# Kernel tuning notes

Hardware: AMD Instinct MI355X
Metric: run time of the kernel (lower is better)

Reference implementation:

```python
import jax, jax.numpy as jnp
import numpy as np

B, N, C, H, P = 16, 4096, 256, 4, 64  # batch, tokens, hidden, heads, proj_size
HD = C // H  # head dim = 64
EPS = 1e-12  # torch F.normalize eps


def _l2norm(t):
    # normalize along last axis, torch-style: t / max(||t||, eps)
    n = jnp.sqrt(jnp.sum(t * t, axis=-1, keepdims=True))
    return t / jnp.maximum(n, EPS)


def setup_inputs() -> dict:
    key = jax.random.key(0)
    ks = jax.random.split(key, 12)
    s = 0.02
    return {
        "x": jax.random.normal(ks[0], (B, N, C), jnp.float32),
        "ref": jax.random.normal(ks[1], (B, N, C), jnp.float32),
        "Wq": jax.random.normal(ks[2], (C, C), jnp.float32) * s,
        "bq": jnp.zeros((C,), jnp.float32),
        "Wkvv": jax.random.normal(ks[3], (3 * C, C), jnp.float32) * s,
        "bkvv": jnp.zeros((3 * C,), jnp.float32),
        "WE": jax.random.normal(ks[4], (P, N), jnp.float32) * s,  # E and F share weights
        "bE": jnp.zeros((P,), jnp.float32),
        "Wo1": jax.random.normal(ks[5], (C // 2, C), jnp.float32) * s,
        "bo1": jnp.zeros((C // 2,), jnp.float32),
        "Wo2": jax.random.normal(ks[6], (C // 2, C), jnp.float32) * s,
        "bo2": jnp.zeros((C // 2,), jnp.float32),
        "temp": jnp.ones((H, 1, 1), jnp.float32),
        "temp2": jnp.ones((H, 1, 1), jnp.float32),
    }


def reference(x, ref, Wq, bq, Wkvv, bkvv, WE, bE, Wo1, bo1, Wo2, bo2, temp, temp2):
    b, n, c = x.shape
    hd = c // H
    # q projection -> [B,H,hd,N] (already transposed so channel dim first)
    q = (x @ Wq.T + bq).reshape(b, n, H, hd).transpose(0, 2, 3, 1)
    kvv = (ref @ Wkvv.T + bkvv).reshape(b, n, 3, H, hd).transpose(2, 0, 3, 4, 1)
    k, v_ca, v_sa = kvv[0], kvv[1], kvv[2]
    # L2 normalize over token axis (last)
    qn = _l2norm(q)
    kn = _l2norm(k)
    # ---- channel attention (XCA-style): [B,H,hd,hd]
    attn_ca = jax.nn.softmax(jnp.einsum('bhcn,bhdn->bhcd', qn, kn) * temp, axis=-1)
    x_ca = jnp.einsum('bhcd,bhdn->bhcn', attn_ca, v_ca)  # [B,H,hd,N]
    x_ca = x_ca.transpose(0, 3, 1, 2).reshape(b, n, c)   # [B,N,C]
    # ---- spatial attention with Linformer-style projection (E == F shared)
    k_proj = kn @ WE.T + bE      # [B,H,hd,P]
    v_proj = v_sa @ WE.T + bE    # [B,H,hd,P]
    attn_sa = jax.nn.softmax(jnp.einsum('bhcn,bhcp->bhnp', qn, k_proj) * temp2, axis=-1)
    x_sa = jnp.einsum('bhnp,bhcp->bhnc', attn_sa, v_proj)  # [B,H,N,hd]
    # faithful to original permute(0,3,1,2).reshape(B,N,C)
    x_sa = x_sa.transpose(0, 3, 1, 2).reshape(b, n, c)
    # output projections + concat (SA first, then CA)
    out_ca = x_ca @ Wo1.T + bo1
    out_sa = x_sa @ Wo2.T + bo2
    return jnp.concatenate((out_sa, out_ca), axis=-1)
```

## Files before the change

### kernel.cpp

```cpp
#include <hip/hip_runtime.h>
#include <hip/hip_bf16.h>

#define DI __device__ __forceinline__

constexpr int B_ = 16, N_ = 4096, C_ = 256, H_ = 4;
constexpr size_t QSZ = (size_t)4096 * 4096;
constexpr int LDW = 72;
constexpr int LDC = 136;

typedef __attribute__((ext_vector_type(8))) short bh8;
typedef __attribute__((ext_vector_type(4))) float fx4;
typedef __attribute__((address_space(1))) unsigned int gu32;
typedef __attribute__((address_space(3))) unsigned int lu32;

DI float bfu2f(unsigned short u) { return __uint_as_float(((unsigned)u) << 16); }
DI void bfu2x2(unsigned u, float& lo, float& hi) {
  lo = __uint_as_float(u << 16);
  hi = __uint_as_float(u & 0xffff0000u);
}
DI unsigned short f2bfu(float f) {
  unsigned u = __float_as_uint(f);
  unsigned r = 0x7fffu + ((u >> 16) & 1u);
  return (unsigned short)((u + r) >> 16);
}
DI void gl_lds16(const unsigned short* g, unsigned short* l) {
  __builtin_amdgcn_global_load_lds((gu32*)g, (lu32*)l, 16, 0, 0);
}

__global__ __launch_bounds__(256) void cast_xref(
    const float* __restrict__ x, const float* __restrict__ ref,
    unsigned short* __restrict__ xb, unsigned short* __restrict__ refb)
{
  const int bid = blockIdx.x;
  const float* src = (bid < 8192) ? x : ref;
  unsigned short* dst = (bid < 8192) ? xb : refb;
  const size_t base = ((size_t)(bid & 8191) * 256 + threadIdx.x) * 8;
  const float4 a = *reinterpret_cast<const float4*>(&src[base]);
  const float4 b = *reinterpret_cast<const float4*>(&src[base + 4]);
  union { uint4 v; unsigned short u[8]; } pk;
  pk.u[0] = f2bfu(a.x); pk.u[1] = f2bfu(a.y); pk.u[2] = f2bfu(a.z); pk.u[3] = f2bfu(a.w);
  pk.u[4] = f2bfu(b.x); pk.u[5] = f2bfu(b.y); pk.u[6] = f2bfu(b.z); pk.u[7] = f2bfu(b.w);
  *reinterpret_cast<uint4*>(&dst[base]) = pk.v;
}

__global__ __launch_bounds__(256) void cast_w(
    const float* __restrict__ Wq, const float* __restrict__ Wkvv,
    const float* __restrict__ Wo2, const float* __restrict__ Wo1,
    const float* __restrict__ WE, unsigned short* __restrict__ Wb,
    unsigned short* __restrict__ wEb)
{
  const int b = blockIdx.x;
  const float* src; unsigned short* dst; int lb;
  if (b < 32)       { src = Wq;   dst = Wb;          lb = b; }
  else if (b < 128) { src = Wkvv; dst = Wb + 65536;  lb = b - 32; }
  else if (b < 144) { src = Wo2;  dst = Wb + 262144; lb = b - 128; }
  else if (b < 160) { src = Wo1;  dst = Wb + 294912; lb = b - 144; }
  else              { src = WE;   dst = wEb;         lb = b - 160; }
  const size_t base = ((size_t)lb * 256 + threadIdx.x) * 8;
  const float4 a = *reinterpret_cast<const float4*>(&src[base]);
  const float4 bb = *reinterpret_cast<const float4*>(&src[base + 4]);
  union { uint4 v; unsigned short u[8]; } pk;
  pk.u[0] = f2bfu(a.x);  pk.u[1] = f2bfu(a.y);  pk.u[2] = f2bfu(a.z);  pk.u[3] = f2bfu(a.w);
  pk.u[4] = f2bfu(bb.x); pk.u[5] = f2bfu(bb.y); pk.u[6] = f2bfu(bb.z); pk.u[7] = f2bfu(bb.w);
  *reinterpret_cast<uint4*>(&dst[base]) = pk.v;
}

__global__ __launch_bounds__(256) void proj_fused(
    const unsigned short* __restrict__ xb, const unsigned short* __restrict__ refb,
    const unsigned short* __restrict__ Wball,
    const float* __restrict__ bq, const float* __restrict__ bkvv,
    unsigned short* __restrict__ qT, unsigned short* __restrict__ kvv2T,
    unsigned short* __restrict__ qtok, unsigned short* __restrict__ vtok)
{
  __shared__ unsigned short smem[32768];
  __shared__ float biasS[128];
  const int tid = threadIdx.x;
  const int lane = tid & 63, wid = tid >> 6;
  const int l15 = lane & 15, l4 = lane >> 4;
  const int wr = wid >> 1, wc = wid & 1;
  const int yt = blockIdx.y;
  const bool isq = (yt < 2);
  const unsigned short* Ab = isq ? xb : refb;
  const unsigned short* Wsrc = isq ? Wball : (Wball + 65536);
  const float* bias = isq ? bq : bkvv;
  unsigned short* outT = isq ? qT : kvv2T;
  const int j0 = (isq ? yt : (yt - 2)) * 128;
  const int pl = j0 >> 8;
  const bool writeT = isq || (pl != 1);
  const int plT = (!isq && pl == 2) ? 1 : 0;
  unsigned short* tok = isq ? qtok : ((pl == 1) ? vtok : nullptr);
  const int n0 = blockIdx.x * 128;
  const int b = blockIdx.z;
  const size_t tok0 = (size_t)b * 4096 + n0;
  const int lrow = lane >> 3, lcb = lane & 7;
  if (tid < 128) biasS[tid] = bias[j0 + tid];

  fx4 acc[4][4];
#pragma unroll
  for (int m = 0; m < 4; ++m)
#pragma unroll
    for (int n = 0; n < 4; ++n) acc[m][n] = (fx4){0.f, 0.f, 0.f, 0.f};

  auto STAGE = [&](int buf, int k0) {
    unsigned short* Wd = smem + buf * 16384;
    unsigned short* Xd = Wd + 8192;
#pragma unroll
    for (int i = 0; i < 4; ++i) {
      const int ci = i * 4 + wid;
      const int row = ci * 8 + lrow;
      const int scb = lcb ^ (row & 7);
      gl_lds16(&Wsrc[(size_t)(j0 + row) * 256 + k0 + scb * 8], &Wd[ci * 512]);
      gl_lds16(&Ab[(tok0 + row) * 256 + k0 + scb * 8], &Xd[ci * 512]);
    }
  };
  auto COMPUTE = [&](int buf) {
    const unsigned short* Ws = smem + buf * 16384;
    const unsigned short* Xs = Ws + 8192;
#pragma unroll
    for (int kk = 0; kk < 2; ++kk) {
      const int cbi = kk * 4 + l4;
      bh8 af[4], bfr[4];
#pragma unroll
      for (int m = 0; m < 4; ++m) {
        const int r = wr * 64 + m * 16 + l15;
        af[m] = *reinterpret_cast<const bh8*>(&Ws[r * 64 + ((cbi ^ (r & 7)) << 3)]);
      }
#pragma unroll
      for (int n = 0; n < 4; ++n) {
        const int r = wc * 64 + n * 16 + l15;
        bfr[n] = *reinterpret_cast<const bh8*>(&Xs[r * 64 + ((cbi ^ (r & 7)) << 3)]);
      }
#pragma unroll
      for (int m = 0; m < 4; ++m)
#pragma unroll
        for (int n = 0; n < 4; ++n)
          acc[m][n] = __builtin_amdgcn_mfma_f32_16x16x32_bf16(af[m], bfr[n], acc[m][n], 0, 0, 0);
    }
  };

  STAGE(0, 0);
  __syncthreads();
  for (int t = 0; t < 4; ++t) {
    if (t < 3) STAGE((t + 1) & 1, (t + 1) * 64);
    COMPUTE(t & 1);
    __syncthreads();
  }

  unsigned short* Co = smem;
#pragma unroll
  for (int m = 0; m < 4; ++m) {
    const int jl = wr * 64 + m * 16 + (l4 << 2);
#pragma unroll
    for (int n = 0; n < 4; ++n) {
      const int col = wc * 64 + n * 16 + l15;
#pragma unroll
      for (int r = 0; r < 4; ++r)
        Co[(jl + r) * LDC + col] = f2bfu(acc[m][n][r] + biasS[jl + r]);
    }
  }
  __syncthreads();
  if (writeT) {
#pragma unroll
    for (int c = 0; c < 8; ++c) {
      const int r = tid >> 1;
      const int colseg = (tid & 1) * 64 + c * 8;
      const uint4 v = *reinterpret_cast<const uint4*>(&Co[r * LDC + colseg]);
      const int jj = j0 + r;
      const int rowT = (plT * B_ + b) * 256 + (jj & 255);
      *reinterpret_cast<uint4*>(&outT[(size_t)rowT * N_ + n0 + colseg]) = v;
    }
  }
  if (tok) {
#pragma unroll
    for (int i = 0; i < 8; ++i) {
      const int idx = i * 256 + tid;
      const int col = idx & 127;
      const int cb = (idx >> 7) * 8;
      union { uint4 v; unsigned short u[8]; } pk;
#pragma unroll
      for (int t = 0; t < 8; ++t) pk.u[t] = Co[(cb + t) * LDC + col];
      const int jj = j0 + cb;
      const int hh = (jj >> 6) & 3, cc = jj & 63;
      *reinterpret_cast<uint4*>(
          &tok[(((size_t)b * 4 + hh) * 4096 + n0 + col) * 64 + cc]) = pk.v;
    }
  }
}

__global__ __launch_bounds__(256) void gemm_outm2(
    const unsigned short* __restrict__ Asa, const unsigned short* __restrict__ Aca,
    const unsigned short* __restrict__ Wob,
    const float* __restrict__ bo2, const float* __restrict__ bo1,
    float* __restrict__ out)
{
  __shared__ unsigned short smem[32768];
  __shared__ float biasS[128];
  const unsigned short* A = (blockIdx.z == 0) ? Asa : Aca;
  const unsigned short* Wsrc = Wob + (size_t)blockIdx.z * 32768;
  const float* bias = (blockIdx.z == 0) ? bo2 : bo1;
  const int joff = blockIdx.z * 128;
  const int tid = threadIdx.x;
  const int lane = tid & 63, wid = tid >> 6;
  const int l15 = lane & 15, l4 = lane >> 4;
  const int wr = wid >> 1, wc = wid & 1;
  const size_t m0 = (size_t)blockIdx.x * 128;
  const int lrow = lane >> 3, lcb = lane & 7;
  if (tid < 128) biasS[tid] = bias[tid];

  fx4 acc[4][4];
#pragma unroll
  for (int m = 0; m < 4; ++m)
#pragma unroll
    for (int n = 0; n < 4; ++n) acc[m][n] = (fx4){0.f, 0.f, 0.f, 0.f};

  auto STAGE = [&](int buf, int k0) {
    unsigned short* Wd = smem + buf * 16384;
    unsigned short* Xd = Wd + 8192;
#pragma unroll
    for (int i = 0; i < 4; ++i) {
      const int ci = i * 4 + wid;
      const int row = ci * 8 + lrow;
      const int scb = lcb ^ (row & 7);
      gl_lds16(&Wsrc[(size_t)row * 256 + k0 + scb * 8], &Wd[ci * 512]);
      gl_lds16(&A[(m0 + row) * 256 + k0 + scb * 8], &Xd[ci * 512]);
    }
  };
  auto COMPUTE = [&](int buf) {
    const unsigned short* Ws = smem + buf * 16384;
    const unsigned short* Xs = Ws + 8192;
#pragma unroll
    for (int kk = 0; kk < 2; ++kk) {
      const int cbi = kk * 4 + l4;
      bh8 af[4], bfr[4];
#pragma unroll
      for (int m = 0; m < 4; ++m) {
        const int r = wr * 64 + m * 16 + l15;
        af[m] = *reinterpret_cast<const bh8*>(&Xs[r * 64 + ((cbi ^ (r & 7)) << 3)]);
      }
#pragma unroll
      for (int n = 0; n < 4; ++n) {
        const int r = wc * 64 + n * 16 + l15;
        bfr[n] = *reinterpret_cast<const bh8*>(&Ws[r * 64 + ((cbi ^ (r & 7)) << 3)]);
      }
#pragma unroll
      for (int m = 0; m < 4; ++m)
#pragma unroll
        for (int n = 0; n < 4; ++n)
          acc[m][n] = __builtin_amdgcn_mfma_f32_16x16x32_bf16(af[m], bfr[n], acc[m][n], 0, 0, 0);
    }
  };

  STAGE(0, 0);
  __syncthreads();
  for (int t = 0; t < 4; ++t) {
    if (t < 3) STAGE((t + 1) & 1, (t + 1) * 64);
    COMPUTE(t & 1);
    __syncthreads();
  }

#pragma unroll
  for (int mi = 0; mi < 4; ++mi) {
    const int mrow = wr * 64 + mi * 16 + (l4 << 2);
#pragma unroll
    for (int ni = 0; ni < 4; ++ni) {
      const int j = wc * 64 + ni * 16 + l15;
      const float bv = biasS[j];
#pragma unroll
      for (int r = 0; r < 4; ++r)
        out[(m0 + mrow + r) * 256 + joff + j] = acc[mi][ni][r] + bv;
    }
  }
}

__global__ __launch_bounds__(256) void norm_kernel(
    const unsigned short* __restrict__ qT, const unsigned short* __restrict__ kT,
    float* __restrict__ rq, float* __restrict__ rk)
{
  const int row = blockIdx.x;
  const unsigned short* src = (row < 4096) ? (qT + (size_t)row * N_)
                                           : (kT + (size_t)(row - 4096) * N_);
  float s = 0.f;
  for (int i = threadIdx.x; i < N_ / 8; i += 256) {
    const uint4 u = *reinterpret_cast<const uint4*>(&src[i * 8]);
    float a, b;
    bfu2x2(u.x, a, b); s += a * a + b * b;
    bfu2x2(u.y, a, b); s += a * a + b * b;
    bfu2x2(u.z, a, b); s += a * a + b * b;
    bfu2x2(u.w, a, b); s += a * a + b * b;
  }
#pragma unroll
  for (int off = 32; off > 0; off >>= 1) s += __shfl_xor(s, off);
  __shared__ float ws4[4];
  if ((threadIdx.x & 63) == 0) ws4[threadIdx.x >> 6] = s;
  __syncthreads();
  if (threadIdx.x == 0) {
    const float tot = ws4[0] + ws4[1] + ws4[2] + ws4[3];
    const float r = 1.f / fmaxf(sqrtf(tot), 1e-12f);
    (row < 4096 ? rq : rk)[row & 4095] = r;
  }
}

__global__ __launch_bounds__(256) void stats_mfma(
    const unsigned short* __restrict__ qT, const unsigned short* __restrict__ kT,
    const unsigned short* __restrict__ vT, const unsigned short* __restrict__ wEb,
    float* __restrict__ part)
{
  __shared__ unsigned short smem[4 * 64 * LDW];
  unsigned short* sq = smem;
  unsigned short* sk = smem + 64 * LDW;
  unsigned short* sv = smem + 2 * 64 * LDW;
  unsigned short* sw = smem + 3 * 64 * LDW;
  const int tid = threadIdx.x;
  const int lane = tid & 63, wid = tid >> 6;
  const int bh = blockIdx.x, chunk = blockIdx.y;
  const size_t rowbase = (size_t)bh * 64 * N_;

  fx4 acc[4][4];
#pragma unroll
  for (int m = 0; m < 4; ++m)
#pragma unroll
    for (int n = 0; n < 4; ++n) acc[m][n] = (fx4){0.f, 0.f, 0.f, 0.f};

  const unsigned short* Aop = (wid == 1) ? sw : (wid == 2) ? sv : sq;
  const unsigned short* Bop = (wid == 1) ? sk : (wid == 2) ? sw : sk;

  for (int tile = 0; tile < 8; ++tile) {
    const int n0 = chunk * 512 + tile * 64;
#pragma unroll
    for (int c = 0; c < 2; ++c) {
      const int idx = c * 256 + tid;
      const int r = idx >> 3;
      const int off = (idx & 7) * 8;
      *reinterpret_cast<uint4*>(&sq[r * LDW + off]) =
          *reinterpret_cast<const uint4*>(&qT[rowbase + (size_t)r * N_ + n0 + off]);
      *reinterpret_cast<uint4*>(&sk[r * LDW + off]) =
          *reinterpret_cast<const uint4*>(&kT[rowbase + (size_t)r * N_ + n0 + off]);
      *reinterpret_cast<uint4*>(&sv[r * LDW + off]) =
          *reinterpret_cast<const uint4*>(&vT[rowbase + (size_t)r * N_ + n0 + off]);
      *reinterpret_cast<uint4*>(&sw[r * LDW + off]) =
          *reinterpret_cast<const uint4*>(&wEb[(size_t)r * N_ + n0 + off]);
    }
    __syncthreads();
    if (wid < 3) {
#pragma unroll
      for (int kk = 0; kk < 2; ++kk) {
        const int kb = kk * 32 + (lane >> 4) * 8;
        bh8 af[4], bfr[4];
#pragma unroll
        for (int m = 0; m < 4; ++m)
          af[m] = *reinterpret_cast<const bh8*>(&Aop[(m * 16 + (lane & 15)) * LDW + kb]);
#pragma unroll
        for (int n = 0; n < 4; ++n)
          bfr[n] = *reinterpret_cast<const bh8*>(&Bop[(n * 16 + (lane & 15)) * LDW + kb]);
#pragma unroll
        for (int m = 0; m < 4; ++m)
#pragma unroll
          for (int n = 0; n < 4; ++n)
            acc[m][n] = __builtin_amdgcn_mfma_f32_16x16x32_bf16(af[m], bfr[n], acc[m][n], 0, 0, 0);
      }
    }
    __syncthreads();
  }

  if (wid < 3) {
    float* base = &part[(((size_t)chunk * 64 + bh) * 3 + wid) * 4096];
#pragma unroll
    for (int m = 0; m < 4; ++m) {
      const int row0 = m * 16 + ((lane >> 4) << 2);
#pragma unroll
      for (int n = 0; n < 4; ++n) {
        const int col = n * 16 + (lane & 15);
#pragma unroll
        for (int r = 0; r < 4; ++r)
          base[(row0 + r) * 64 + col] = acc[m][n][r];
      }
    }
  }
}

__global__ __launch_bounds__(256) void postproc_kernel(
    const float* __restrict__ part, const float* __restrict__ rq,
    const float* __restrict__ rk, const float* __restrict__ bE,
    const float* __restrict__ temp, const float* __restrict__ temp2,
    unsigned short* __restrict__ attn_b,
    unsigned short* __restrict__ kp2t, unsigned short* __restrict__ vpb)
{
  __shared__ float sums[12288];
  const int bh = blockIdx.x;
  const int tid = threadIdx.x;
  for (int idx = tid; idx < 12288; idx += 256) {
    float s = 0.f;
    for (int ch = 0; ch < 8; ++ch)
      s += part[((size_t)ch * 64 + bh) * 12288 + idx];
    sums[idx] = s;
  }
  __syncthreads();
  const float t2 = temp2[bh & 3];
  for (int idx = tid; idx < 4096; idx += 256) {
    const int p = idx >> 6, c = idx & 63;
    kp2t[(size_t)bh * 4096 + idx] =
        f2bfu((sums[4096 + idx] * rk[bh * 64 + c] + bE[p]) * rq[bh * 64 + c] * t2);
    vpb[(size_t)bh * 4096 + idx] = f2bfu(sums[8192 + idx] + bE[idx & 63]);
  }
  const float tv = temp[bh & 3];
  const int lane = tid & 63, wv = tid >> 6;
  for (int ri = 0; ri < 16; ++ri) {
    const int c = wv * 16 + ri;
    const float val = sums[c * 64 + lane] * rq[bh * 64 + c] * rk[bh * 64 + lane] * tv;
    float m = val;
#pragma unroll
    for (int off = 32; off > 0; off >>= 1) m = fmaxf(m, __shfl_xor(m, off));
    const float e = __expf(val - m);
    float ssum = e;
#pragma unroll
    for (int off = 32; off > 0; off >>= 1) ssum += __shfl_xor(ssum, off);
    attn_b[(size_t)bh * 4096 + c * 64 + lane] = f2bfu(e / ssum);
  }
}

__global__ __launch_bounds__(256) void sa_mfma(
    const unsigned short* __restrict__ qtok, const unsigned short* __restrict__ kp2t,
    const unsigned short* __restrict__ vpb, unsigned short* __restrict__ x_sa)
{
  __shared__ unsigned short skp[64 * LDW];
  __shared__ unsigned short svp[64 * LDW];
  __shared__ unsigned short pt[4][64 * LDW];
  const int tid = threadIdx.x;
  const int lane = tid & 63, wid = tid >> 6;
  const int l15 = lane & 15, l4 = lane >> 4;
  const int bh = blockIdx.x, b = bh >> 2, h = bh & 3;
  const int n0 = blockIdx.y * 256 + wid * 64;
  unsigned short* myp = &pt[wid][0];

#pragma unroll
  for (int i = 0; i < 2; ++i) {
    const int idx = i * 256 + tid;
    const int r = idx >> 3, off = (idx & 7) * 8;
    *reinterpret_cast<uint4*>(&skp[r * LDW + off]) =
        *reinterpret_cast<const uint4*>(&kp2t[(size_t)bh * 4096 + r * 64 + off]);
    *reinterpret_cast<uint4*>(&svp[r * LDW + off]) =
        *reinterpret_cast<const uint4*>(&vpb[(size_t)bh * 4096 + r * 64 + off]);
  }
  __syncthreads();

  fx4 acc[4][4];
#pragma unroll
  for (int m = 0; m < 4; ++m)
#pragma unroll
    for (int j = 0; j < 4; ++j) acc[m][j] = (fx4){0.f, 0.f, 0.f, 0.f};
  const size_t qbase = ((size_t)bh * 4096 + n0) * 64;
#pragma unroll
  for (int kk = 0; kk < 2; ++kk) {
    const int kb = kk * 32 + l4 * 8;
    bh8 af[4], bf[4];
#pragma unroll
    for (int m = 0; m < 4; ++m)
      af[m] = *reinterpret_cast<const bh8*>(&qtok[qbase + (size_t)(m * 16 + l15) * 64 + kb]);
#pragma unroll
    for (int j = 0; j < 4; ++j)
      bf[j] = *reinterpret_cast<const bh8*>(&skp[(j * 16 + l15) * LDW + kb]);
#pragma unroll
    for (int m = 0; m < 4; ++m)
#pragma unroll
      for (int j = 0; j < 4; ++j)
        acc[m][j] = __builtin_amdgcn_mfma_f32_16x16x32_bf16(af[m], bf[j], acc[m][j], 0, 0, 0);
  }

  fx4 inv[4];
#pragma unroll
  for (int m = 0; m < 4; ++m) {
    fx4 vm = acc[m][0];
#pragma unroll
    for (int j = 1; j < 4; ++j)
#pragma unroll
      for (int r = 0; r < 4; ++r) vm[r] = fmaxf(vm[r], acc[m][j][r]);
#pragma unroll
    for (int msk = 1; msk < 16; msk <<= 1)
#pragma unroll
      for (int r = 0; r < 4; ++r) vm[r] = fmaxf(vm[r], __shfl_xor(vm[r], msk));
    fx4 s = (fx4){0.f, 0.f, 0.f, 0.f};
#pragma unroll
    for (int j = 0; j < 4; ++j)
#pragma unroll
      for (int r = 0; r < 4; ++r) {
        acc[m][j][r] = __expf(acc[m][j][r] - vm[r]);
        s[r] += acc[m][j][r];
      }
#pragma unroll
    for (int msk = 1; msk < 16; msk <<= 1)
#pragma unroll
      for (int r = 0; r < 4; ++r) s[r] += __shfl_xor(s[r], msk);
#pragma unroll
    for (int r = 0; r < 4; ++r) inv[m][r] = 1.f / s[r];
#pragma unroll
    for (int j = 0; j < 4; ++j)
#pragma unroll
      for (int r = 0; r < 4; ++r)
        myp[(m * 16 + l4 * 4 + r) * LDW + j * 16 + l15] = f2bfu(acc[m][j][r]);
  }

  fx4 acc2[4][4];
#pragma unroll
  for (int m = 0; m < 4; ++m)
#pragma unroll
    for (int j = 0; j < 4; ++j) acc2[m][j] = (fx4){0.f, 0.f, 0.f, 0.f};
#pragma unroll
  for (int kk = 0; kk < 2; ++kk) {
    const int kb = kk * 32 + l4 * 8;
    bh8 af[4], bf[4];
#pragma unroll
    for (int m = 0; m < 4; ++m)
      af[m] = *reinterpret_cast<const bh8*>(&myp[(m * 16 + l15) * LDW + kb]);
#pragma unroll
    for (int j = 0; j < 4; ++j)
      bf[j] = *reinterpret_cast<const bh8*>(&svp[(j * 16 + l15) * LDW + kb]);
#pragma unroll
    for (int m = 0; m < 4; ++m)
#pragma unroll
      for (int j = 0; j < 4; ++j)
        acc2[m][j] = __builtin_amdgcn_mfma_f32_16x16x32_bf16(af[m], bf[j], acc2[m][j], 0, 0, 0);
  }

#pragma unroll
  for (int m = 0; m < 4; ++m)
#pragma unroll
    for (int j = 0; j < 4; ++j)
#pragma unroll
      for (int r = 0; r < 4; ++r)
        myp[(m * 16 + l4 * 4 + r) * 65 + j * 16 + l15] = f2bfu(acc2[m][j][r] * inv[m][r]);
#pragma unroll
  for (int dstep = 0; dstep < 8; ++dstep) {
    const int d = dstep * 8 + (lane >> 3);
    const int nseg = (lane & 7) * 8;
    union { uint4 v; unsigned short u[8]; } pk;
#pragma unroll
    for (int t = 0; t < 8; ++t) pk.u[t] = myp[(nseg + t) * 65 + d];
    *reinterpret_cast<uint4*>(
        &x_sa[((size_t)(b * 64 + d) * 4 + h) * (size_t)N_ + n0 + nseg]) = pk.v;
  }
}

__global__ __launch_bounds__(256) void xca_mfma(
    const unsigned short* __restrict__ attn_b, const unsigned short* __restrict__ vtok,
    unsigned short* __restrict__ x_ca)
{
  __shared__ unsigned short co[4][64 * LDW];
  const int tid = threadIdx.x;
  const int lane = tid & 63, wid = tid >> 6;
  const int l15 = lane & 15, l4 = lane >> 4;
  const int bh = blockIdx.x, b = bh >> 2, h = bh & 3;
  const int n0 = blockIdx.y * 256 + wid * 64;
  unsigned short* myco = &co[wid][0];

  fx4 acc[4][4];
#pragma unroll
  for (int m = 0; m < 4; ++m)
#pragma unroll
    for (int j = 0; j < 4; ++j) acc[m][j] = (fx4){0.f, 0.f, 0.f, 0.f};
  const size_t abase = (size_t)bh * 4096;
  const size_t vbase = ((size_t)bh * 4096 + n0) * 64;
#pragma unroll
  for (int kk = 0; kk < 2; ++kk) {
    const int kb = kk * 32 + l4 * 8;
    bh8 af[4], bf[4];
#pragma unroll
    for (int m = 0; m < 4; ++m)
      af[m] = *reinterpret_cast<const bh8*>(&attn_b[abase + (size_t)(m * 16 + l15) * 64 + kb]);
#pragma unroll
    for (int j = 0; j < 4; ++j)
      bf[j] = *reinterpret_cast<const bh8*>(&vtok[vbase + (size_t)(j * 16 + l15) * 64 + kb]);
#pragma unroll
    for (int m = 0; m < 4; ++m)
#pragma unroll
      for (int j = 0; j < 4; ++j)
        acc[m][j] = __builtin_amdgcn_mfma_f32_16x16x32_bf16(af[m], bf[j], acc[m][j], 0, 0, 0);
  }

#pragma unroll
  for (int m = 0; m < 4; ++m)
#pragma unroll
    for (int j = 0; j < 4; ++j)
#pragma unroll
      for (int r = 0; r < 4; ++r)
        myco[(j * 16 + l15) * LDW + m * 16 + l4 * 4 + r] = f2bfu(acc[m][j][r]);
#pragma unroll
  for (int p = 0; p < 8; ++p) {
    const int nloc = p * 8 + (lane >> 3);
    const int cseg = (lane & 7) * 8;
    const uint4 v = *reinterpret_cast<const uint4*>(&myco[nloc * LDW + cseg]);
    *reinterpret_cast<uint4*>(
        &x_ca[((size_t)b * N_ + n0 + nloc) * 256 + h * 64 + cseg]) = v;
  }
}

extern "C" void kernel_launch(void* const* d_in, const int* in_sizes, int n_in,
                              void* d_out, int out_size, void* d_ws, size_t ws_size,
                              hipStream_t stream)
{
  const float* x     = (const float*)d_in[0];
  const float* ref   = (const float*)d_in[1];
  const float* Wq    = (const float*)d_in[2];
  const float* bq    = (const float*)d_in[3];
  const float* Wkvv  = (const float*)d_in[4];
  const float* bkvv  = (const float*)d_in[5];
  const float* WE    = (const float*)d_in[6];
  const float* bE    = (const float*)d_in[7];
  const float* Wo1   = (const float*)d_in[8];
  const float* bo1   = (const float*)d_in[9];
  const float* Wo2   = (const float*)d_in[10];
  const float* bo2   = (const float*)d_in[11];
  const float* temp  = (const float*)d_in[12];
  const float* temp2 = (const float*)d_in[13];
  float* out = (float*)d_out;

  char* ws = (char*)d_ws;
  unsigned short* qT      = (unsigned short*)(ws);
  unsigned short* kvv2T   = (unsigned short*)(ws + 33554432);
  unsigned short* qtok    = (unsigned short*)(ws + 100663296);
  unsigned short* refb    = (unsigned short*)(ws + 134217728);
  unsigned short* x_sa    = (unsigned short*)(ws + 134217728);
  unsigned short* vca_tok = (unsigned short*)(ws + 167772160);
  unsigned short* xb      = (unsigned short*)(ws + 201326592);
  float*          part    = (float*)(ws + 201326592);
  unsigned short* x_ca    = (unsigned short*)(ws + 201326592);
  unsigned short* Wb      = (unsigned short*)(ws + 234881024);
  unsigned short* wEb     = (unsigned short*)(ws + 235536384);
  float* rq     = (float*)(ws + 236060672);
  float* rk     = (float*)(ws + 236077056);
  unsigned short* attn_b  = (unsigned short*)(ws + 236093440);
  unsigned short* kp2t    = (unsigned short*)(ws + 236617728);
  unsigned short* vpb     = (unsigned short*)(ws + 237142016);

  const dim3 blk(256);
  cast_xref<<<dim3(16384), blk, 0, stream>>>(x, ref, xb, refb);
  cast_w<<<dim3(288), blk, 0, stream>>>(Wq, Wkvv, Wo2, Wo1, WE, Wb, wEb);
  proj_fused<<<dim3(32, 8, 16), blk, 0, stream>>>(xb, refb, Wb, bq, bkvv,
                                                  qT, kvv2T, qtok, vca_tok);
  norm_kernel<<<dim3(8192), blk, 0, stream>>>(qT, kvv2T, rq, rk);
  stats_mfma<<<dim3(64, 8), blk, 0, stream>>>(qT, kvv2T, kvv2T + QSZ, wEb, part);
  postproc_kernel<<<dim3(64), blk, 0, stream>>>(part, rq, rk, bE, temp, temp2,
                                                attn_b, kp2t, vpb);
  sa_mfma<<<dim3(64, 16), blk, 0, stream>>>(qtok, kp2t, vpb, x_sa);
  xca_mfma<<<dim3(64, 16), blk, 0, stream>>>(attn_b, vca_tok, x_ca);
  gemm_outm2<<<dim3(512, 1, 2), blk, 0, stream>>>(x_sa, x_ca, Wb + 262144, bo2, bo1, out);
}
```

Before: 242.9 us.

## Fuse L2 norm reduction into stats kernel and coalesce projection epilogue stores

Removes the standalone norm kernel, which re-read all of q and k (about 64 MB of bf16), and computes the squared sums in the idle fourth wave of stats_mfma from tiles already staged in shared memory. Per-chunk partial norms go to a small partN buffer and are reduced in postproc. The proj_fused epilogue stores are also remapped so that each row write is 256 contiguous bytes and the token-layout writes cover adjacent tokens. The extra work in wave 3 could lengthen each stats iteration, and partN must not overlap other live workspace regions.

```diff
diff --git a/kernel.cpp b/kernel.cpp
--- a/kernel.cpp
+++ b/kernel.cpp
@@ -162,8 +162,8 @@
   if (writeT) {
 #pragma unroll
     for (int c = 0; c < 8; ++c) {
-      const int r = tid >> 1;
-      const int colseg = (tid & 1) * 64 + c * 8;
+      const int r = c * 16 + (tid >> 4);
+      const int colseg = (tid & 15) * 8;
       const uint4 v = *reinterpret_cast<const uint4*>(&Co[r * LDC + colseg]);
       const int jj = j0 + r;
       const int rowT = (plT * B_ + b) * 256 + (jj & 255);
@@ -173,16 +173,16 @@
   if (tok) {
 #pragma unroll
     for (int i = 0; i < 8; ++i) {
-      const int idx = i * 256 + tid;
-      const int col = idx & 127;
-      const int cb = (idx >> 7) * 8;
+      const int half = i >> 2;
+      const int cb = half * 64 + (tid & 7) * 8;
+      const int nloc = (i & 3) * 32 + (tid >> 3);
       union { uint4 v; unsigned short u[8]; } pk;
 #pragma unroll
-      for (int t = 0; t < 8; ++t) pk.u[t] = Co[(cb + t) * LDC + col];
+      for (int t = 0; t < 8; ++t) pk.u[t] = Co[(cb + t) * LDC + nloc];
       const int jj = j0 + cb;
       const int hh = (jj >> 6) & 3, cc = jj & 63;
       *reinterpret_cast<uint4*>(
-          &tok[(((size_t)b * 4 + hh) * 4096 + n0 + col) * 64 + cc]) = pk.v;
+          &tok[(((size_t)b * 4 + hh) * 4096 + n0 + nloc) * 64 + cc]) = pk.v;
     }
   }
 }
@@ -272,38 +272,10 @@
   }
 }
 
-__global__ __launch_bounds__(256) void norm_kernel(
-    const unsigned short* __restrict__ qT, const unsigned short* __restrict__ kT,
-    float* __restrict__ rq, float* __restrict__ rk)
-{
-  const int row = blockIdx.x;
-  const unsigned short* src = (row < 4096) ? (qT + (size_t)row * N_)
-                                           : (kT + (size_t)(row - 4096) * N_);
-  float s = 0.f;
-  for (int i = threadIdx.x; i < N_ / 8; i += 256) {
-    const uint4 u = *reinterpret_cast<const uint4*>(&src[i * 8]);
-    float a, b;
-    bfu2x2(u.x, a, b); s += a * a + b * b;
-    bfu2x2(u.y, a, b); s += a * a + b * b;
-    bfu2x2(u.z, a, b); s += a * a + b * b;
-    bfu2x2(u.w, a, b); s += a * a + b * b;
-  }
-#pragma unroll
-  for (int off = 32; off > 0; off >>= 1) s += __shfl_xor(s, off);
-  __shared__ float ws4[4];
-  if ((threadIdx.x & 63) == 0) ws4[threadIdx.x >> 6] = s;
-  __syncthreads();
-  if (threadIdx.x == 0) {
-    const float tot = ws4[0] + ws4[1] + ws4[2] + ws4[3];
-    const float r = 1.f / fmaxf(sqrtf(tot), 1e-12f);
-    (row < 4096 ? rq : rk)[row & 4095] = r;
-  }
-}
-
 __global__ __launch_bounds__(256) void stats_mfma(
     const unsigned short* __restrict__ qT, const unsigned short* __restrict__ kT,
     const unsigned short* __restrict__ vT, const unsigned short* __restrict__ wEb,
-    float* __restrict__ part)
+    float* __restrict__ part, float* __restrict__ partN)
 {
   __shared__ unsigned short smem[4 * 64 * LDW];
   unsigned short* sq = smem;
@@ -320,6 +292,7 @@
   for (int m = 0; m < 4; ++m)
 #pragma unroll
     for (int n = 0; n < 4; ++n) acc[m][n] = (fx4){0.f, 0.f, 0.f, 0.f};
+  float q2 = 0.f, k2 = 0.f;
 
   const unsigned short* Aop = (wid == 1) ? sw : (wid == 2) ? sv : sq;
   const unsigned short* Bop = (wid == 1) ? sk : (wid == 2) ? sw : sk;
@@ -358,6 +331,23 @@
           for (int n = 0; n < 4; ++n)
             acc[m][n] = __builtin_amdgcn_mfma_f32_16x16x32_bf16(af[m], bfr[n], acc[m][n], 0, 0, 0);
       }
+    } else {
+      const unsigned short* qrow = &sq[lane * LDW];
+      const unsigned short* krow = &sk[lane * LDW];
+#pragma unroll
+      for (int t = 0; t < 8; ++t) {
+        const uint4 uq = *reinterpret_cast<const uint4*>(&qrow[t * 8]);
+        const uint4 uk = *reinterpret_cast<const uint4*>(&krow[t * 8]);
+        float a, b;
+        bfu2x2(uq.x, a, b); q2 += a * a + b * b;
+        bfu2x2(uq.y, a, b); q2 += a * a + b * b;
+        bfu2x2(uq.z, a, b); q2 += a * a + b * b;
+        bfu2x2(uq.w, a, b); q2 += a * a + b * b;
+        bfu2x2(uk.x, a, b); k2 += a * a + b * b;
+        bfu2x2(uk.y, a, b); k2 += a * a + b * b;
+        bfu2x2(uk.z, a, b); k2 += a * a + b * b;
+        bfu2x2(uk.w, a, b); k2 += a * a + b * b;
+      }
     }
     __syncthreads();
   }
@@ -375,17 +365,22 @@
           base[(row0 + r) * 64 + col] = acc[m][n][r];
       }
     }
+  } else {
+    float* nb = &partN[((size_t)chunk * 64 + bh) * 128];
+    nb[lane] = q2;
+    nb[64 + lane] = k2;
   }
 }
 
 __global__ __launch_bounds__(256) void postproc_kernel(
-    const float* __restrict__ part, const float* __restrict__ rq,
-    const float* __restrict__ rk, const float* __restrict__ bE,
+    const float* __restrict__ part, const float* __restrict__ partN,
+    const float* __restrict__ bE,
     const float* __restrict__ temp, const float* __restrict__ temp2,
     unsigned short* __restrict__ attn_b,
     unsigned short* __restrict__ kp2t, unsigned short* __restrict__ vpb)
 {
   __shared__ float sums[12288];
+  __shared__ float rqS[64], rkS[64];
   const int bh = blockIdx.x;
   const int tid = threadIdx.x;
   for (int idx = tid; idx < 12288; idx += 256) {
@@ -394,19 +389,26 @@
       s += part[((size_t)ch * 64 + bh) * 12288 + idx];
     sums[idx] = s;
   }
+  if (tid < 128) {
+    float s = 0.f;
+    for (int ch = 0; ch < 8; ++ch)
+      s += partN[((size_t)ch * 64 + bh) * 128 + tid];
+    const float r = 1.f / fmaxf(sqrtf(s), 1e-12f);
+    if (tid < 64) rqS[tid] = r; else rkS[tid - 64] = r;
+  }
   __syncthreads();
   const float t2 = temp2[bh & 3];
   for (int idx = tid; idx < 4096; idx += 256) {
     const int p = idx >> 6, c = idx & 63;
     kp2t[(size_t)bh * 4096 + idx] =
-        f2bfu((sums[4096 + idx] * rk[bh * 64 + c] + bE[p]) * rq[bh * 64 + c] * t2);
+        f2bfu((sums[4096 + idx] * rkS[c] + bE[p]) * rqS[c] * t2);
     vpb[(size_t)bh * 4096 + idx] = f2bfu(sums[8192 + idx] + bE[idx & 63]);
   }
   const float tv = temp[bh & 3];
   const int lane = tid & 63, wv = tid >> 6;
   for (int ri = 0; ri < 16; ++ri) {
     const int c = wv * 16 + ri;
-    const float val = sums[c * 64 + lane] * rq[bh * 64 + c] * rk[bh * 64 + lane] * tv;
+    const float val = sums[c * 64 + lane] * rqS[c] * rkS[lane] * tv;
     float m = val;
 #pragma unroll
     for (int off = 32; off > 0; off >>= 1) m = fmaxf(m, __shfl_xor(m, off));
@@ -623,10 +625,9 @@
   unsigned short* xb      = (unsigned short*)(ws + 201326592);
   float*          part    = (float*)(ws + 201326592);
   unsigned short* x_ca    = (unsigned short*)(ws + 201326592);
+  float*          partN   = (float*)(ws + 226492416);
   unsigned short* Wb      = (unsigned short*)(ws + 234881024);
   unsigned short* wEb     = (unsigned short*)(ws + 235536384);
-  float* rq     = (float*)(ws + 236060672);
-  float* rk     = (float*)(ws + 236077056);
   unsigned short* attn_b  = (unsigned short*)(ws + 236093440);
   unsigned short* kp2t    = (unsigned short*)(ws + 236617728);
   unsigned short* vpb     = (unsigned short*)(ws + 237142016);
@@ -636,9 +637,8 @@
   cast_w<<<dim3(288), blk, 0, stream>>>(Wq, Wkvv, Wo2, Wo1, WE, Wb, wEb);
   proj_fused<<<dim3(32, 8, 16), blk, 0, stream>>>(xb, refb, Wb, bq, bkvv,
                                                   qT, kvv2T, qtok, vca_tok);
-  norm_kernel<<<dim3(8192), blk, 0, stream>>>(qT, kvv2T, rq, rk);
-  stats_mfma<<<dim3(64, 8), blk, 0, stream>>>(qT, kvv2T, kvv2T + QSZ, wEb, part);
-  postproc_kernel<<<dim3(64), blk, 0, stream>>>(part, rq, rk, bE, temp, temp2,
+  stats_mfma<<<dim3(64, 8), blk, 0, stream>>>(qT, kvv2T, kvv2T + QSZ, wEb, part, partN);
+  postproc_kernel<<<dim3(64), blk, 0, stream>>>(part, partN, bE, temp, temp2,
                                                 attn_b, kp2t, vpb);
   sa_mfma<<<dim3(64, 16), blk, 0, stream>>>(qtok, kp2t, vpb, x_sa);
   xca_mfma<<<dim3(64, 16), blk, 0, stream>>>(attn_b, vca_tok, x_ca);
```

Result: faster. 213.4 us (-12.1%).
